# Optimization experiments

Hardware: AMD Instinct MI355X
Metric: run time of the kernel (lower is better)

## Reference

```python
import jax, jax.numpy as jnp
import numpy as np

N_NODES = 50000
N_EDGES = 800000
D = 128
N_LAYERS = 3
N_GRAPHS = 256


def setup_inputs() -> dict:
    key = jax.random.key(0)
    ks = jax.random.split(key, 6)
    x = jax.random.normal(ks[0], (N_NODES, D), dtype=jnp.float32)
    edge_index = jax.random.randint(ks[1], (2, N_EDGES), 0, N_NODES, dtype=jnp.int64)
    batch = jnp.sort(jax.random.randint(ks[2], (N_NODES,), 0, N_GRAPHS, dtype=jnp.int64))
    # Xavier-uniform linear weights (bias filled with 0 per weights_init)
    limit = float(np.sqrt(6.0 / (D + D)))
    W1 = jax.random.uniform(ks[3], (N_LAYERS, D, D), jnp.float32, -limit, limit)
    W2 = jax.random.uniform(ks[4], (N_LAYERS, D, D), jnp.float32, -limit, limit)
    b1 = jnp.zeros((N_LAYERS, D), jnp.float32)
    b2 = jnp.zeros((N_LAYERS, D), jnp.float32)
    return {"x": x, "edge_index": edge_index, "batch": batch,
            "W1": W1, "b1": b1, "W2": W2, "b2": b2}


def reference(x, edge_index, batch, W1, b1, W2, b2):
    src, dst = edge_index[0], edge_index[1]
    h = x  # [N, D]
    pools = []
    for i in range(N_LAYERS):
        # GINConv, eps=0: (1+eps)*h + sum of neighbor (source) features at target
        agg = jax.ops.segment_sum(h[src], dst, num_segments=N_NODES)  # [N, D]
        h = h + agg
        # MLP: Linear -> ReLU -> Linear, then outer ReLU activation
        h = jnp.maximum(h @ W1[i] + b1[i], 0.0) @ W2[i] + b2[i]
        h = jnp.maximum(h, 0.0)
        # global_add_pool over graph ids
        pools.append(jax.ops.segment_sum(h, batch, num_segments=N_GRAPHS))
    return jnp.concatenate(pools, axis=1)  # [N_GRAPHS, N_LAYERS*D]
```

## Files before the change

### kernel.cpp

```cpp
#include <hip/hip_runtime.h>

#define N_NODES 50000
#define N_EDGES 800000
#define DIM 128
#define N_LAYERS 3
#define N_GRAPHS 256
#define OUT_COLS (N_LAYERS * DIM)

#define SUBS 4
#define SUBCAP 24
#define ROWSTRIDE (SUBS * SUBCAP)

#define FILL_NB 3125
#define X2H_NB 6250
#define WPREP_NB 384

typedef __attribute__((ext_vector_type(8))) _Float16 half8;
typedef __attribute__((ext_vector_type(4))) float f32x4;
typedef __attribute__((ext_vector_type(4))) unsigned short us4;
typedef __attribute__((ext_vector_type(8))) short short8;

__global__ __launch_bounds__(256) void prep_kernel(
        const int* __restrict__ src, const int* __restrict__ dst,
        int* __restrict__ deg4, unsigned short* __restrict__ elist,
        const float* __restrict__ x, unsigned short* __restrict__ x16,
        const float* __restrict__ W1, const float* __restrict__ W2,
        _Float16* __restrict__ Wt) {
    const int b = blockIdx.x;
    if (b < FILL_NB) {
        int e = b * 256 + threadIdx.x;
        int d = dst[e];
        int s = src[e];
        int sub = e & (SUBS - 1);
        int r = atomicAdd(&deg4[d * SUBS + sub], 1);
        if (r < SUBCAP) elist[(size_t)d * ROWSTRIDE + sub * SUBCAP + r] = (unsigned short)s;
    } else if (b < FILL_NB + X2H_NB) {
        int i = (b - FILL_NB) * 256 + threadIdx.x;
        float4 v = *(const float4*)&x[(size_t)i * 4];
        us4 o;
        _Float16 h0 = (_Float16)v.x, h1 = (_Float16)v.y, h2 = (_Float16)v.z, h3 = (_Float16)v.w;
        o.x = *(unsigned short*)&h0; o.y = *(unsigned short*)&h1;
        o.z = *(unsigned short*)&h2; o.w = *(unsigned short*)&h3;
        *(us4*)&x16[(size_t)i * 4] = o;
    } else {
        int i = (b - FILL_NB - X2H_NB) * 256 + threadIdx.x;
        int which = i / (N_LAYERS * DIM * DIM);
        int rem = i % (N_LAYERS * DIM * DIM);
        int layer = rem / (DIM * DIM);
        int kj = rem % (DIM * DIM);
        int k = kj / DIM, j = kj % DIM;
        float w = (which ? W2 : W1)[rem];
        int lin = layer * 2 + which;
        Wt[(lin * DIM + j) * DIM + k] = (_Float16)w;
    }
}

__global__ __launch_bounds__(256) void gather_kernel(
        const unsigned short* __restrict__ hin, const int* __restrict__ deg4,
        const unsigned short* __restrict__ elist,
        unsigned short* __restrict__ agg) {
    int node = (blockIdx.x * blockDim.x + threadIdx.x) >> 5;
    int lane = threadIdx.x & 31;
    if (node >= N_NODES) return;
    union H4 { uint2 u; _Float16 h[4]; };
    const size_t rb = (size_t)node * DIM + lane * 4;
    H4 s;
    s.u = *(const uint2*)&hin[rb];
    float a0 = (float)s.h[0], a1 = (float)s.h[1], a2 = (float)s.h[2], a3 = (float)s.h[3];
    int4 c4 = *(const int4*)&deg4[node * SUBS];
#pragma unroll
    for (int sub = 0; sub < SUBS; sub++) {
        int cnt = ((const int*)&c4)[sub];
        if (cnt > SUBCAP) cnt = SUBCAP;
        const unsigned short* el = &elist[(size_t)node * ROWSTRIDE + sub * SUBCAP];
        int i = 0;
        for (; i + 4 <= cnt; i += 4) {
            int e0 = el[i], e1 = el[i + 1], e2 = el[i + 2], e3 = el[i + 3];
            H4 v0, v1, v2, v3;
            v0.u = *(const uint2*)&hin[(size_t)e0 * DIM + lane * 4];
            v1.u = *(const uint2*)&hin[(size_t)e1 * DIM + lane * 4];
            v2.u = *(const uint2*)&hin[(size_t)e2 * DIM + lane * 4];
            v3.u = *(const uint2*)&hin[(size_t)e3 * DIM + lane * 4];
            a0 += ((float)v0.h[0] + (float)v1.h[0]) + ((float)v2.h[0] + (float)v3.h[0]);
            a1 += ((float)v0.h[1] + (float)v1.h[1]) + ((float)v2.h[1] + (float)v3.h[1]);
            a2 += ((float)v0.h[2] + (float)v1.h[2]) + ((float)v2.h[2] + (float)v3.h[2]);
            a3 += ((float)v0.h[3] + (float)v1.h[3]) + ((float)v2.h[3] + (float)v3.h[3]);
        }
        for (; i < cnt; i++) {
            H4 v0;
            v0.u = *(const uint2*)&hin[(size_t)el[i] * DIM + lane * 4];
            a0 += (float)v0.h[0];
            a1 += (float)v0.h[1];
            a2 += (float)v0.h[2];
            a3 += (float)v0.h[3];
        }
    }
    _Float16 h0 = (_Float16)a0, h1 = (_Float16)a1, h2 = (_Float16)a2, h3 = (_Float16)a3;
    uint2 oh;
    oh.x = (unsigned)*(unsigned short*)&h0 | ((unsigned)*(unsigned short*)&h1 << 16);
    oh.y = (unsigned)*(unsigned short*)&h2 | ((unsigned)*(unsigned short*)&h3 << 16);
    *(uint2*)&agg[rb] = oh;
}

__global__ __launch_bounds__(64, 4) void mlp_pool_wave_kernel(
        const unsigned short* __restrict__ Agg,
        const _Float16* __restrict__ Wt,
        const float* __restrict__ bias1, const float* __restrict__ bias2,
        const int* __restrict__ batch, unsigned short* __restrict__ h16out,
        float* __restrict__ pool_out, int layer, int write_h) {
    __shared__ float S[16][132];
    __shared__ int gb[16];
    const int l = threadIdx.x;
    const int lr = l & 15;
    const int lk = l >> 4;
    const int row0 = blockIdx.x * 16;

    if (l < 16) gb[l] = batch[row0 + l];

    const size_t ab = (size_t)(row0 + lr) * DIM + lk * 8;
    half8 ah[4];
#pragma unroll
    for (int kb = 0; kb < 4; kb++) ah[kb] = *(const half8*)&Agg[ab + kb * 32];

#pragma unroll
    for (int cb = 0; cb < 8; cb++) {
        const _Float16* wp = &Wt[(cb * 16 + lr) * DIM + lk * 8];
        half8 w[4];
#pragma unroll
        for (int kb = 0; kb < 4; kb++) w[kb] = *(const half8*)&wp[kb * 32];
        f32x4 aA = {0.f, 0.f, 0.f, 0.f};
#pragma unroll
        for (int kb = 0; kb < 4; kb++)
            aA = __builtin_amdgcn_mfma_f32_16x16x32_f16(ah[kb], w[kb], aA, 0, 0, 0);
        float bv = bias1[cb * 16 + lr];
#pragma unroll
        for (int r = 0; r < 4; r++)
            S[lk * 4 + r][cb * 16 + lr] = fmaxf(aA[r] + bv, 0.f);
    }

    half8 ch[4], cl[4];
#pragma unroll
    for (int kb = 0; kb < 4; kb++) {
        const float* sr = &S[lr][kb * 32 + lk * 8];
        f32x4 u0 = *(const f32x4*)&sr[0];
        f32x4 u1 = *(const f32x4*)&sr[4];
        float uu[8] = {u0.x, u0.y, u0.z, u0.w, u1.x, u1.y, u1.z, u1.w};
        half8 hh, ll;
#pragma unroll
        for (int j = 0; j < 8; j++) {
            _Float16 hv = (_Float16)uu[j];
            hh[j] = hv;
            ll[j] = (_Float16)(uu[j] - (float)hv);
        }
        ch[kb] = hh;
        cl[kb] = ll;
    }

    const _Float16* W2 = Wt + DIM * DIM;
#pragma unroll
    for (int cb = 0; cb < 8; cb++) {
        const _Float16* wp = &W2[(cb * 16 + lr) * DIM + lk * 8];
        half8 w[4];
#pragma unroll
        for (int kb = 0; kb < 4; kb++) w[kb] = *(const half8*)&wp[kb * 32];
        f32x4 aA = {0.f, 0.f, 0.f, 0.f}, aC = aA;
#pragma unroll
        for (int kb = 0; kb < 4; kb++) {
            aA = __builtin_amdgcn_mfma_f32_16x16x32_f16(ch[kb], w[kb], aA, 0, 0, 0);
            aC = __builtin_amdgcn_mfma_f32_16x16x32_f16(cl[kb], w[kb], aC, 0, 0, 0);
        }
        float bv = bias2[cb * 16 + lr];
#pragma unroll
        for (int r = 0; r < 4; r++)
            S[lk * 4 + r][cb * 16 + lr] = fmaxf(aA[r] + aC[r] + bv, 0.f);
    }

    if (write_h) {
        const int r = l >> 2, c0 = (l & 3) * 32;
        unsigned short buf[32];
#pragma unroll
        for (int j = 0; j < 32; j++) {
            _Float16 hv = (_Float16)S[r][c0 + j];
            buf[j] = *(unsigned short*)&hv;
        }
        const size_t ob = (size_t)(row0 + r) * DIM + c0;
#pragma unroll
        for (int q = 0; q < 4; q++)
            *(short8*)&h16out[ob + q * 8] = *(const short8*)&buf[q * 8];
    }

    const int d0 = 2 * l;
    float p0 = 0.f, p1 = 0.f;
    int curg = gb[0];
    for (int r = 0; r < 16; r++) {
        int g = gb[r];
        if (g != curg) {
            atomicAdd(&pool_out[curg * OUT_COLS + layer * DIM + d0], p0);
            atomicAdd(&pool_out[curg * OUT_COLS + layer * DIM + d0 + 1], p1);
            p0 = p1 = 0.f;
            curg = g;
        }
        p0 += S[r][d0];
        p1 += S[r][d0 + 1];
    }
    atomicAdd(&pool_out[curg * OUT_COLS + layer * DIM + d0], p0);
    atomicAdd(&pool_out[curg * OUT_COLS + layer * DIM + d0 + 1], p1);
}


extern "C" void kernel_launch(void* const* d_in, const int* in_sizes, int n_in,
                              void* d_out, int out_size, void* d_ws, size_t ws_size,
                              hipStream_t stream) {
    const float* x = (const float*)d_in[0];
    const int* ei = (const int*)d_in[1];
    const int* batch = (const int*)d_in[2];
    const float* W1 = (const float*)d_in[3];
    const float* b1 = (const float*)d_in[4];
    const float* W2 = (const float*)d_in[5];
    const float* b2 = (const float*)d_in[6];
    float* out = (float*)d_out;

    const int* src = ei;
    const int* dst = ei + N_EDGES;

    char* ws = (char*)d_ws;
    unsigned short* buf0 = (unsigned short*)ws;
    unsigned short* agg = (unsigned short*)(ws + 12800000);
    int* deg4 = (int*)(ws + 25600000);
    _Float16* Wt = (_Float16*)(ws + 26400000);
    unsigned short* elist = (unsigned short*)(ws + 26596608);

    hipMemsetAsync(d_out, 0, (size_t)out_size * sizeof(float), stream);
    hipMemsetAsync(deg4, 0, (size_t)N_NODES * SUBS * sizeof(int), stream);

    prep_kernel<<<FILL_NB + X2H_NB + WPREP_NB, 256, 0, stream>>>(
        src, dst, deg4, elist, x, buf0, W1, W2, Wt);

    const int gather_grid = (N_NODES * 32 + 255) / 256;
    const int mlp_grid = N_NODES / 16;

    for (int layer = 0; layer < N_LAYERS; layer++) {
        gather_kernel<<<gather_grid, 256, 0, stream>>>(buf0, deg4, elist, agg);
        mlp_pool_wave_kernel<<<mlp_grid, 64, 0, stream>>>(
            agg, Wt + (size_t)layer * 2 * DIM * DIM,
            b1 + layer * DIM, b2 + layer * DIM, batch, buf0, out, layer,
            (layer < N_LAYERS - 1) ? 1 : 0);
    }
}
```

Baseline: 284.2 us.

## Fuse neighbor gather into per-layer MLP+pool kernel with ping-pong buffers

```diff
diff --git a/kernel.cpp b/kernel.cpp
--- a/kernel.cpp
+++ b/kernel.cpp
@@ -55,55 +55,9 @@
     }
 }
 
-__global__ __launch_bounds__(256) void gather_kernel(
+__global__ __launch_bounds__(64, 4) void fused_layer_kernel(
         const unsigned short* __restrict__ hin, const int* __restrict__ deg4,
         const unsigned short* __restrict__ elist,
-        unsigned short* __restrict__ agg) {
-    int node = (blockIdx.x * blockDim.x + threadIdx.x) >> 5;
-    int lane = threadIdx.x & 31;
-    if (node >= N_NODES) return;
-    union H4 { uint2 u; _Float16 h[4]; };
-    const size_t rb = (size_t)node * DIM + lane * 4;
-    H4 s;
-    s.u = *(const uint2*)&hin[rb];
-    float a0 = (float)s.h[0], a1 = (float)s.h[1], a2 = (float)s.h[2], a3 = (float)s.h[3];
-    int4 c4 = *(const int4*)&deg4[node * SUBS];
-#pragma unroll
-    for (int sub = 0; sub < SUBS; sub++) {
-        int cnt = ((const int*)&c4)[sub];
-        if (cnt > SUBCAP) cnt = SUBCAP;
-        const unsigned short* el = &elist[(size_t)node * ROWSTRIDE + sub * SUBCAP];
-        int i = 0;
-        for (; i + 4 <= cnt; i += 4) {
-            int e0 = el[i], e1 = el[i + 1], e2 = el[i + 2], e3 = el[i + 3];
-            H4 v0, v1, v2, v3;
-            v0.u = *(const uint2*)&hin[(size_t)e0 * DIM + lane * 4];
-            v1.u = *(const uint2*)&hin[(size_t)e1 * DIM + lane * 4];
-            v2.u = *(const uint2*)&hin[(size_t)e2 * DIM + lane * 4];
-            v3.u = *(const uint2*)&hin[(size_t)e3 * DIM + lane * 4];
-            a0 += ((float)v0.h[0] + (float)v1.h[0]) + ((float)v2.h[0] + (float)v3.h[0]);
-            a1 += ((float)v0.h[1] + (float)v1.h[1]) + ((float)v2.h[1] + (float)v3.h[1]);
-            a2 += ((float)v0.h[2] + (float)v1.h[2]) + ((float)v2.h[2] + (float)v3.h[2]);
-            a3 += ((float)v0.h[3] + (float)v1.h[3]) + ((float)v2.h[3] + (float)v3.h[3]);
-        }
-        for (; i < cnt; i++) {
-            H4 v0;
-            v0.u = *(const uint2*)&hin[(size_t)el[i] * DIM + lane * 4];
-            a0 += (float)v0.h[0];
-            a1 += (float)v0.h[1];
-            a2 += (float)v0.h[2];
-            a3 += (float)v0.h[3];
-        }
-    }
-    _Float16 h0 = (_Float16)a0, h1 = (_Float16)a1, h2 = (_Float16)a2, h3 = (_Float16)a3;
-    uint2 oh;
-    oh.x = (unsigned)*(unsigned short*)&h0 | ((unsigned)*(unsigned short*)&h1 << 16);
-    oh.y = (unsigned)*(unsigned short*)&h2 | ((unsigned)*(unsigned short*)&h3 << 16);
-    *(uint2*)&agg[rb] = oh;
-}
-
-__global__ __launch_bounds__(64, 4) void mlp_pool_wave_kernel(
-        const unsigned short* __restrict__ Agg,
         const _Float16* __restrict__ Wt,
         const float* __restrict__ bias1, const float* __restrict__ bias2,
         const int* __restrict__ batch, unsigned short* __restrict__ h16out,
@@ -117,10 +71,57 @@
 
     if (l < 16) gb[l] = batch[row0 + l];
 
-    const size_t ab = (size_t)(row0 + lr) * DIM + lk * 8;
+    const int node = row0 + lr;
+    float acc[4][8];
+    {
+        const size_t sb = (size_t)node * DIM + lk * 8;
+#pragma unroll
+        for (int kb = 0; kb < 4; kb++) {
+            half8 v = *(const half8*)&hin[sb + kb * 32];
+#pragma unroll
+            for (int j = 0; j < 8; j++) acc[kb][j] = (float)v[j];
+        }
+    }
+    int4 c4 = *(const int4*)&deg4[node * SUBS];
+    const unsigned short* elbase = &elist[(size_t)node * ROWSTRIDE];
+#pragma unroll
+    for (int sub = 0; sub < SUBS; sub++) {
+        int cnt = ((const int*)&c4)[sub];
+        if (cnt > SUBCAP) cnt = SUBCAP;
+        const unsigned short* el = elbase + sub * SUBCAP;
+        int i = 0;
+        for (; i + 2 <= cnt; i += 2) {
+            int s0 = el[i], s1 = el[i + 1];
+            const size_t b0 = (size_t)s0 * DIM + lk * 8;
+            const size_t b1 = (size_t)s1 * DIM + lk * 8;
+            half8 v0[4], v1[4];
+#pragma unroll
+            for (int kb = 0; kb < 4; kb++) {
+                v0[kb] = *(const half8*)&hin[b0 + kb * 32];
+                v1[kb] = *(const half8*)&hin[b1 + kb * 32];
+            }
+#pragma unroll
+            for (int kb = 0; kb < 4; kb++)
+#pragma unroll
+                for (int j = 0; j < 8; j++)
+                    acc[kb][j] += (float)v0[kb][j] + (float)v1[kb][j];
+        }
+        if (i < cnt) {
+            int s0 = el[i];
+            const size_t b0 = (size_t)s0 * DIM + lk * 8;
+#pragma unroll
+            for (int kb = 0; kb < 4; kb++) {
+                half8 v0 = *(const half8*)&hin[b0 + kb * 32];
+#pragma unroll
+                for (int j = 0; j < 8; j++) acc[kb][j] += (float)v0[j];
+            }
+        }
+    }
     half8 ah[4];
 #pragma unroll
-    for (int kb = 0; kb < 4; kb++) ah[kb] = *(const half8*)&Agg[ab + kb * 32];
+    for (int kb = 0; kb < 4; kb++)
+#pragma unroll
+        for (int j = 0; j < 8; j++) ah[kb][j] = (_Float16)acc[kb][j];
 
 #pragma unroll
     for (int cb = 0; cb < 8; cb++) {
@@ -224,26 +225,27 @@
     const int* dst = ei + N_EDGES;
 
     char* ws = (char*)d_ws;
-    unsigned short* buf0 = (unsigned short*)ws;
-    unsigned short* agg = (unsigned short*)(ws + 12800000);
-    int* deg4 = (int*)(ws + 25600000);
-    _Float16* Wt = (_Float16*)(ws + 26400000);
-    unsigned short* elist = (unsigned short*)(ws + 26596608);
+    unsigned short* x16 = (unsigned short*)ws;
+    unsigned short* hA = (unsigned short*)(ws + 12800000);
+    unsigned short* hB = (unsigned short*)(ws + 25600000);
+    int* deg4 = (int*)(ws + 38400000);
+    _Float16* Wt = (_Float16*)(ws + 39200000);
+    unsigned short* elist = (unsigned short*)(ws + 39396608);
 
     hipMemsetAsync(d_out, 0, (size_t)out_size * sizeof(float), stream);
     hipMemsetAsync(deg4, 0, (size_t)N_NODES * SUBS * sizeof(int), stream);
 
     prep_kernel<<<FILL_NB + X2H_NB + WPREP_NB, 256, 0, stream>>>(
-        src, dst, deg4, elist, x, buf0, W1, W2, Wt);
-
-    const int gather_grid = (N_NODES * 32 + 255) / 256;
-    const int mlp_grid = N_NODES / 16;
-
+        src, dst, deg4, elist, x, x16, W1, W2, Wt);
+
+    const int grid = N_NODES / 16;
+
+    const unsigned short* hin[3] = {x16, hA, hB};
+    unsigned short* hout[3] = {hA, hB, nullptr};
     for (int layer = 0; layer < N_LAYERS; layer++) {
-        gather_kernel<<<gather_grid, 256, 0, stream>>>(buf0, deg4, elist, agg);
-        mlp_pool_wave_kernel<<<mlp_grid, 64, 0, stream>>>(
-            agg, Wt + (size_t)layer * 2 * DIM * DIM,
-            b1 + layer * DIM, b2 + layer * DIM, batch, buf0, out, layer,
+        fused_layer_kernel<<<grid, 64, 0, stream>>>(
+            hin[layer], deg4, elist, Wt + (size_t)layer * 2 * DIM * DIM,
+            b1 + layer * DIM, b2 + layer * DIM, batch, hout[layer], out, layer,
             (layer < N_LAYERS - 1) ? 1 : 0);
     }
 }
```

Result: faster. 242.6 us, median of 2 (-14.6%).
